# Kernel tuning notes

Hardware: AMD Instinct MI355X
Metric: run time of the kernel (lower is better)

## Reference

```python
import jax, jax.numpy as jnp
import numpy as np

B, T, D, O, E = 4, 4096, 256, 256, 16


def setup_inputs() -> dict:
    key = jax.random.key(0)
    ks = jax.random.split(key, 5)
    s_in = 1.0 / np.sqrt(D)
    x = jax.random.normal(ks[0], (B, T, D), dtype=jnp.float32)
    We = jax.random.uniform(ks[1], (E, D, O), minval=-s_in, maxval=s_in, dtype=jnp.float32)
    be = jax.random.uniform(ks[2], (E, O), minval=-s_in, maxval=s_in, dtype=jnp.float32)
    Wg = jax.random.uniform(ks[3], (D, E), minval=-s_in, maxval=s_in, dtype=jnp.float32)
    bg = jax.random.uniform(ks[4], (E,), minval=-s_in, maxval=s_in, dtype=jnp.float32)
    return {"x": x, "We": We, "be": be, "Wg": Wg, "bg": bg}


def reference(x, We, be, Wg, bg):
    # gate: softmax over experts  [B,T,E]
    gate = jax.nn.softmax(jnp.einsum("btd,de->bte", x, Wg) + bg, axis=-1)
    # all experts: batched GEMM  [B,T,E,O]
    h = jax.nn.gelu(jnp.einsum("btd,edo->bteo", x, We) + be, approximate=False)
    # softmax-weighted sum over experts  [B,T,O]
    return jnp.einsum("bteo,bte->bto", h, gate)
```

## Files before the change

kernel.cpp:

```cpp
#include <hip/hip_runtime.h>
#include <stdint.h>

#define KD 256
#define NO 256
#define NE 16
#define BM 64
#define BN 128
#define XROW 264
#define GROW 68

typedef short bf16x8 __attribute__((ext_vector_type(8)));
typedef float f32x4 __attribute__((ext_vector_type(4)));

__device__ __forceinline__ unsigned short f2bf(float f) {
  uint32_t u = __float_as_uint(f);
  u += 0x7fffu + ((u >> 16) & 1u);
  return (unsigned short)(u >> 16);
}
__device__ __forceinline__ float bf2f(unsigned short h) {
  return __uint_as_float(((uint32_t)h) << 16);
}
__device__ __forceinline__ float gelu_f(float h) {
#if __has_builtin(__builtin_amdgcn_exp2f)
  float zn = h * fmaf(-0.10294817f, h * h, -2.3022077f);
  return h * __builtin_amdgcn_rcpf(1.0f + __builtin_amdgcn_exp2f(zn));
#else
  float z = h * fmaf(0.07135481627f, h * h, 1.5957691216f);
  return h * __builtin_amdgcn_rcpf(1.0f + __expf(-z));
#endif
}

__device__ __forceinline__ void dma16(const void* g, void* l) {
  __builtin_amdgcn_global_load_lds(
      (const __attribute__((address_space(1))) uint32_t*)g,
      (__attribute__((address_space(3))) uint32_t*)l, 16, 0, 0);
}

__global__ void moe_prep(const float* __restrict__ We, unsigned short* __restrict__ Wf,
                         const float* __restrict__ Wg, unsigned short* __restrict__ Wgt)
{
  const int tid = threadIdx.x;
  const int bid = blockIdx.x;
  const int w = tid >> 6, lane = tid & 63;
  const int g = bid * 4 + w;
  const int e = g >> 7, kc = (g >> 4) & 7, ob = g & 15;
  const int q = lane >> 4, ln = lane & 15;

  const float* src = We + ((size_t)e * KD + kc * 32 + q * 8) * NO + ob * 16 + ln;
  unsigned int pk[4];
#pragma unroll
  for (int h = 0; h < 4; ++h) {
    unsigned short lo = f2bf(src[(h * 2 + 0) * NO]);
    unsigned short hi = f2bf(src[(h * 2 + 1) * NO]);
    pk[h] = (unsigned int)lo | ((unsigned int)hi << 16);
  }
  uint4* dst = (uint4*)(Wf + ((((size_t)(e * 8 + kc) * 16 + ob) * 64) + lane) * 8);
  *dst = make_uint4(pk[0], pk[1], pk[2], pk[3]);

  if (bid == 0) {
    int d = tid;
    const float* wr = Wg + (size_t)d * NE;
#pragma unroll
    for (int ee = 0; ee < NE; ++ee)
      Wgt[ee * KD + d] = f2bf(wr[ee]);
  }
}

__launch_bounds__(256, 1)
__global__ void moe_main(const float* __restrict__ x,
                         const uint4* __restrict__ Wf,
                         const unsigned short* __restrict__ Wgt,
                         const float* __restrict__ be,
                         const float* __restrict__ bg,
                         float* __restrict__ out)
{
  __shared__ __align__(16) unsigned char BB[131072];
  __shared__ __align__(16) float gate_t[NE * GROW];
  __shared__ unsigned short be_h[NE * BN];

  unsigned short* const Xs = (unsigned short*)BB;

  const int tid = threadIdx.x;
  const int bid = blockIdx.x;
  const int half = bid & 1;
  const int n0 = half * BN;
  const int m0 = (bid >> 1) * BM;
  const int w = tid >> 6, lane = tid & 63;
  const int ln = lane & 15, quad = lane >> 4;
  const int eoff = __builtin_amdgcn_readfirstlane(((tid >> 6) * 4 + bid) & 15);
  const int obb = half * 8 + w * 2;

  {
    const float4* xg = (const float4*)x + (size_t)m0 * (KD / 4);
#pragma unroll
    for (int p = 0; p < 16; ++p) {
      int idx = p * 256 + tid;
      int r = idx >> 6, c = idx & 63;
      float4 v = xg[r * (KD / 4) + c];
      uint32_t lo = (uint32_t)f2bf(v.x) | ((uint32_t)f2bf(v.y) << 16);
      uint32_t hi = (uint32_t)f2bf(v.z) | ((uint32_t)f2bf(v.w) << 16);
      *(uint2*)&Xs[r * XROW + c * 4] = make_uint2(lo, hi);
    }
  }
#pragma unroll
  for (int p = 0; p < 8; ++p) {
    int idx = p * 256 + tid;
    int e = idx >> 7, c = idx & 127;
    be_h[e * BN + c] = f2bf(be[e * NO + n0 + c]);
  }
  __syncthreads();

  bf16x8 a[4][8];
#pragma unroll
  for (int i = 0; i < 4; ++i)
#pragma unroll
    for (int kc = 0; kc < 8; ++kc)
      a[i][kc] = *(const bf16x8*)&Xs[(i * 16 + ln) * XROW + kc * 32 + quad * 8];

  {
    f32x4 g = {0.f, 0.f, 0.f, 0.f};
#pragma unroll
    for (int kc = 0; kc < 8; ++kc) {
      bf16x8 af = *(const bf16x8*)&Xs[(w * 16 + ln) * XROW + kc * 32 + quad * 8];
      bf16x8 wb = *(const bf16x8*)(Wgt + (size_t)ln * KD + kc * 32 + quad * 8);
      g = __builtin_amdgcn_mfma_f32_16x16x32_bf16(af, wb, g, 0, 0, 0);
    }
    float bgl = bg[ln];
#pragma unroll
    for (int r = 0; r < 4; ++r) {
      float v = g[r] + bgl;
      float mx = v;
#pragma unroll
      for (int msk = 1; msk < 16; msk <<= 1)
        mx = fmaxf(mx, __shfl_xor(mx, msk, 64));
      float ev = __expf(v - mx);
      float s = ev;
#pragma unroll
      for (int msk = 1; msk < 16; msk <<= 1)
        s += __shfl_xor(s, msk, 64);
      gate_t[ln * GROW + w * 16 + quad * 4 + r] = ev * __builtin_amdgcn_rcpf(s);
    }
  }
  __syncthreads();

  const char* const WfB = (const char*)Wf;
  char* const slab0 = (char*)BB + w * 32768;
  char* const slab1 = slab0 + 16384;
  {
    const char* s0 = WfB + (size_t)eoff * 131072 + (size_t)obb * 1024 + lane * 16;
    const char* s1 = WfB + (size_t)((eoff + 1) & 15) * 131072 + (size_t)obb * 1024 + lane * 16;
#pragma unroll
    for (int s = 0; s < 16; ++s)
      dma16(s0 + (s >> 1) * 16384 + (s & 1) * 1024, slab0 + s * 1024 + lane * 16);
#pragma unroll
    for (int s = 0; s < 16; ++s)
      dma16(s1 + (s >> 1) * 16384 + (s & 1) * 1024, slab1 + s * 1024 + lane * 16);
  }

  f32x4 acc[4][2], oacc[4][2];
#pragma unroll
  for (int i = 0; i < 4; ++i)
#pragma unroll
    for (int j = 0; j < 2; ++j) {
      acc[i][j] = (f32x4){0.f, 0.f, 0.f, 0.f};
      oacc[i][j] = (f32x4){0.f, 0.f, 0.f, 0.f};
    }

#pragma unroll 1
  for (int ei = 0; ei < NE; ++ei) {
    const int e = (eoff + ei) & 15;

    if (ei < NE - 1) {
      asm volatile("s_waitcnt vmcnt(16)" ::: "memory");
    } else {
      asm volatile("s_waitcnt vmcnt(0)" ::: "memory");
    }
    __builtin_amdgcn_sched_barrier(0);

    char* const cur = (ei & 1) ? slab1 : slab0;
#pragma unroll
    for (int kc = 0; kc < 8; ++kc) {
      const bf16x8 b0 = *(const bf16x8*)(cur + (kc * 2 + 0) * 1024 + lane * 16);
      const bf16x8 b1 = *(const bf16x8*)(cur + (kc * 2 + 1) * 1024 + lane * 16);
#pragma unroll
      for (int i = 0; i < 4; ++i) {
        acc[i][0] = __builtin_amdgcn_mfma_f32_16x16x32_bf16(a[i][kc], b0, acc[i][0], 0, 0, 0);
        acc[i][1] = __builtin_amdgcn_mfma_f32_16x16x32_bf16(a[i][kc], b1, acc[i][1], 0, 0, 0);
      }
    }

    if (ei < NE - 2) {
      const int en2 = (eoff + ei + 2) & 15;
      const char* sn = WfB + (size_t)en2 * 131072 + (size_t)obb * 1024 + lane * 16;
#pragma unroll
      for (int s = 0; s < 16; ++s)
        dma16(sn + (s >> 1) * 16384 + (s & 1) * 1024, cur + s * 1024 + lane * 16);
    }

    {
      f32x4 gv[4];
#pragma unroll
      for (int i = 0; i < 4; ++i)
        gv[i] = *(const f32x4*)&gate_t[e * GROW + i * 16 + quad * 4];
      const float bb0 = bf2f(be_h[e * BN + w * 32 + ln]);
      const float bb1 = bf2f(be_h[e * BN + w * 32 + 16 + ln]);
#pragma unroll
      for (int i = 0; i < 4; ++i)
#pragma unroll
        for (int j = 0; j < 2; ++j)
#pragma unroll
          for (int r = 0; r < 4; ++r) {
            float hh = acc[i][j][r] + (j ? bb1 : bb0);
            oacc[i][j][r] = fmaf(gv[i][r], gelu_f(hh), oacc[i][j][r]);
            acc[i][j][r] = 0.f;
          }
    }
  }

#pragma unroll
  for (int i = 0; i < 4; ++i)
#pragma unroll
    for (int r = 0; r < 4; ++r) {
      int row = m0 + i * 16 + quad * 4 + r;
      float* orow = out + (size_t)row * NO + n0 + w * 32 + ln;
      orow[0]  = oacc[i][0][r];
      orow[16] = oacc[i][1][r];
    }
}

extern "C" void kernel_launch(void* const* d_in, const int* in_sizes, int n_in,
                              void* d_out, int out_size, void* d_ws, size_t ws_size,
                              hipStream_t stream) {
  const float* x  = (const float*)d_in[0];
  const float* We = (const float*)d_in[1];
  const float* be = (const float*)d_in[2];
  const float* Wg = (const float*)d_in[3];
  const float* bg = (const float*)d_in[4];
  float* out = (float*)d_out;
  unsigned short* Wf  = (unsigned short*)d_ws;
  unsigned short* Wgt = (unsigned short*)((char*)d_ws + (size_t)NE * NO * KD * 2);

  moe_prep<<<512, 256, 0, stream>>>(We, Wf, Wg, Wgt);
  moe_main<<<512, 256, 0, stream>>>(x, (const uint4*)Wf, Wgt, be, bg, out);
}
```

Baseline: 137.3 us.

## Retile MoE kernel to 128x64 blocks with shared cooperative weight slabs

Block tile changes from 64x128 to 128x64, so each wave now owns 32 rows across all 64 columns instead of 64 rows across 32 columns. Expert weight slabs in LDS become shared by all waves, loaded cooperatively (each wave DMAs two k-chunks), which cuts per-block LDS to about 67KB and allows two blocks per CU. This needs workgroup barriers around each expert's compute. B fragments are register double-buffered across k-chunks to hide LDS latency. The trade is less x reuse per weight load and extra barrier sync.

Result: faster. 127.5 us (-7.1%).

```diff
diff --git a/kernel.cpp b/kernel.cpp
--- a/kernel.cpp
+++ b/kernel.cpp
@@ -4,10 +4,10 @@
 #define KD 256
 #define NO 256
 #define NE 16
-#define BM 64
-#define BN 128
+#define BM 128
+#define BN 64
 #define XROW 264
-#define GROW 68
+#define GROW 132
 
 typedef short bf16x8 __attribute__((ext_vector_type(8)));
 typedef float f32x4 __attribute__((ext_vector_type(4)));
@@ -66,7 +66,7 @@
   }
 }
 
-__launch_bounds__(256, 1)
+__launch_bounds__(256, 2)
 __global__ void moe_main(const float* __restrict__ x,
                          const uint4* __restrict__ Wf,
                          const unsigned short* __restrict__ Wgt,
@@ -74,26 +74,26 @@
                          const float* __restrict__ bg,
                          float* __restrict__ out)
 {
-  __shared__ __align__(16) unsigned char BB[131072];
+  __shared__ __align__(16) unsigned char BB[BM * XROW * 2];
   __shared__ __align__(16) float gate_t[NE * GROW];
   __shared__ unsigned short be_h[NE * BN];
 
-  unsigned short* const Xs = (unsigned short*)BB;
-
   const int tid = threadIdx.x;
   const int bid = blockIdx.x;
-  const int half = bid & 1;
-  const int n0 = half * BN;
-  const int m0 = (bid >> 1) * BM;
+  const int cq = bid & 3;
+  const int n0 = cq * BN;
+  const int m0 = (bid >> 2) * BM;
   const int w = tid >> 6, lane = tid & 63;
   const int ln = lane & 15, quad = lane >> 4;
-  const int eoff = __builtin_amdgcn_readfirstlane(((tid >> 6) * 4 + bid) & 15);
-  const int obb = half * 8 + w * 2;
+  const int eoff = __builtin_amdgcn_readfirstlane(bid & 15);
+  const int obBase = cq * 4;
+
+  unsigned short* const Xs = (unsigned short*)BB;
 
   {
     const float4* xg = (const float4*)x + (size_t)m0 * (KD / 4);
 #pragma unroll
-    for (int p = 0; p < 16; ++p) {
+    for (int p = 0; p < 32; ++p) {
       int idx = p * 256 + tid;
       int r = idx >> 6, c = idx & 63;
       float4 v = xg[r * (KD / 4) + c];
@@ -103,25 +103,27 @@
     }
   }
 #pragma unroll
-  for (int p = 0; p < 8; ++p) {
+  for (int p = 0; p < 4; ++p) {
     int idx = p * 256 + tid;
-    int e = idx >> 7, c = idx & 127;
+    int e = idx >> 6, c = idx & 63;
     be_h[e * BN + c] = f2bf(be[e * NO + n0 + c]);
   }
   __syncthreads();
 
-  bf16x8 a[4][8];
-#pragma unroll
-  for (int i = 0; i < 4; ++i)
+  bf16x8 a[2][8];
+#pragma unroll
+  for (int i = 0; i < 2; ++i)
 #pragma unroll
     for (int kc = 0; kc < 8; ++kc)
-      a[i][kc] = *(const bf16x8*)&Xs[(i * 16 + ln) * XROW + kc * 32 + quad * 8];
-
-  {
+      a[i][kc] = *(const bf16x8*)&Xs[(w * 32 + i * 16 + ln) * XROW + kc * 32 + quad * 8];
+
+#pragma unroll
+  for (int pass = 0; pass < 2; ++pass) {
+    const int rw = w * 2 + pass;
     f32x4 g = {0.f, 0.f, 0.f, 0.f};
 #pragma unroll
     for (int kc = 0; kc < 8; ++kc) {
-      bf16x8 af = *(const bf16x8*)&Xs[(w * 16 + ln) * XROW + kc * 32 + quad * 8];
+      bf16x8 af = *(const bf16x8*)&Xs[(rw * 16 + ln) * XROW + kc * 32 + quad * 8];
       bf16x8 wb = *(const bf16x8*)(Wgt + (size_t)ln * KD + kc * 32 + quad * 8);
       g = __builtin_amdgcn_mfma_f32_16x16x32_bf16(af, wb, g, 0, 0, 0);
     }
@@ -138,93 +140,118 @@
 #pragma unroll
       for (int msk = 1; msk < 16; msk <<= 1)
         s += __shfl_xor(s, msk, 64);
-      gate_t[ln * GROW + w * 16 + quad * 4 + r] = ev * __builtin_amdgcn_rcpf(s);
+      gate_t[ln * GROW + rw * 16 + quad * 4 + r] = ev * __builtin_amdgcn_rcpf(s);
     }
   }
   __syncthreads();
 
+  char* const slab0 = (char*)BB;
+  char* const slab1 = (char*)BB + 32768;
   const char* const WfB = (const char*)Wf;
-  char* const slab0 = (char*)BB + w * 32768;
-  char* const slab1 = slab0 + 16384;
   {
-    const char* s0 = WfB + (size_t)eoff * 131072 + (size_t)obb * 1024 + lane * 16;
-    const char* s1 = WfB + (size_t)((eoff + 1) & 15) * 131072 + (size_t)obb * 1024 + lane * 16;
-#pragma unroll
-    for (int s = 0; s < 16; ++s)
-      dma16(s0 + (s >> 1) * 16384 + (s & 1) * 1024, slab0 + s * 1024 + lane * 16);
-#pragma unroll
-    for (int s = 0; s < 16; ++s)
-      dma16(s1 + (s >> 1) * 16384 + (s & 1) * 1024, slab1 + s * 1024 + lane * 16);
-  }
-
-  f32x4 acc[4][2], oacc[4][2];
-#pragma unroll
-  for (int i = 0; i < 4; ++i)
-#pragma unroll
-    for (int j = 0; j < 2; ++j) {
-      acc[i][j] = (f32x4){0.f, 0.f, 0.f, 0.f};
-      oacc[i][j] = (f32x4){0.f, 0.f, 0.f, 0.f};
+    const int e1 = (eoff + 1) & 15;
+#pragma unroll
+    for (int s = 0; s < 8; ++s) {
+      const int kc = w * 2 + (s >> 2), jf = s & 3;
+      dma16(WfB + ((size_t)((eoff * 8 + kc) * 16 + obBase + jf)) * 1024 + lane * 16,
+            slab0 + (kc * 4 + jf) * 1024 + lane * 16);
+    }
+#pragma unroll
+    for (int s = 0; s < 8; ++s) {
+      const int kc = w * 2 + (s >> 2), jf = s & 3;
+      dma16(WfB + ((size_t)((e1 * 8 + kc) * 16 + obBase + jf)) * 1024 + lane * 16,
+            slab1 + (kc * 4 + jf) * 1024 + lane * 16);
+    }
+  }
+
+  f32x4 acc[2][4], oacc[2][4];
+#pragma unroll
+  for (int i = 0; i < 2; ++i)
+#pragma unroll
+    for (int jf = 0; jf < 4; ++jf) {
+      acc[i][jf] = (f32x4){0.f, 0.f, 0.f, 0.f};
+      oacc[i][jf] = (f32x4){0.f, 0.f, 0.f, 0.f};
     }
 
 #pragma unroll 1
   for (int ei = 0; ei < NE; ++ei) {
     const int e = (eoff + ei) & 15;
+    char* const cur = (ei & 1) ? slab1 : slab0;
 
     if (ei < NE - 1) {
-      asm volatile("s_waitcnt vmcnt(16)" ::: "memory");
+      asm volatile("s_waitcnt vmcnt(8)" ::: "memory");
     } else {
       asm volatile("s_waitcnt vmcnt(0)" ::: "memory");
     }
     __builtin_amdgcn_sched_barrier(0);
-
-    char* const cur = (ei & 1) ? slab1 : slab0;
+    __builtin_amdgcn_s_barrier();
+    __builtin_amdgcn_sched_barrier(0);
+
+    bf16x8 bq0[4], bq1[4];
+#pragma unroll
+    for (int jf = 0; jf < 4; ++jf)
+      bq0[jf] = *(const bf16x8*)(cur + jf * 1024 + lane * 16);
 #pragma unroll
     for (int kc = 0; kc < 8; ++kc) {
-      const bf16x8 b0 = *(const bf16x8*)(cur + (kc * 2 + 0) * 1024 + lane * 16);
-      const bf16x8 b1 = *(const bf16x8*)(cur + (kc * 2 + 1) * 1024 + lane * 16);
-#pragma unroll
-      for (int i = 0; i < 4; ++i) {
-        acc[i][0] = __builtin_amdgcn_mfma_f32_16x16x32_bf16(a[i][kc], b0, acc[i][0], 0, 0, 0);
-        acc[i][1] = __builtin_amdgcn_mfma_f32_16x16x32_bf16(a[i][kc], b1, acc[i][1], 0, 0, 0);
+      const bf16x8* cu = (kc & 1) ? bq1 : bq0;
+      bf16x8* nx = (kc & 1) ? bq0 : bq1;
+      if (kc < 7) {
+#pragma unroll
+        for (int jf = 0; jf < 4; ++jf)
+          nx[jf] = *(const bf16x8*)(cur + ((kc + 1) * 4 + jf) * 1024 + lane * 16);
       }
-    }
+#pragma unroll
+      for (int i = 0; i < 2; ++i)
+#pragma unroll
+        for (int jf = 0; jf < 4; ++jf)
+          acc[i][jf] = __builtin_amdgcn_mfma_f32_16x16x32_bf16(
+              a[i][kc], cu[jf], acc[i][jf], 0, 0, 0);
+    }
+
+    __builtin_amdgcn_sched_barrier(0);
+    __builtin_amdgcn_s_barrier();
+    __builtin_amdgcn_sched_barrier(0);
 
     if (ei < NE - 2) {
       const int en2 = (eoff + ei + 2) & 15;
-      const char* sn = WfB + (size_t)en2 * 131072 + (size_t)obb * 1024 + lane * 16;
-#pragma unroll
-      for (int s = 0; s < 16; ++s)
-        dma16(sn + (s >> 1) * 16384 + (s & 1) * 1024, cur + s * 1024 + lane * 16);
+#pragma unroll
+      for (int s = 0; s < 8; ++s) {
+        const int kc = w * 2 + (s >> 2), jf = s & 3;
+        dma16(WfB + ((size_t)((en2 * 8 + kc) * 16 + obBase + jf)) * 1024 + lane * 16,
+              cur + (kc * 4 + jf) * 1024 + lane * 16);
+      }
     }
 
     {
-      f32x4 gv[4];
-#pragma unroll
-      for (int i = 0; i < 4; ++i)
-        gv[i] = *(const f32x4*)&gate_t[e * GROW + i * 16 + quad * 4];
-      const float bb0 = bf2f(be_h[e * BN + w * 32 + ln]);
-      const float bb1 = bf2f(be_h[e * BN + w * 32 + 16 + ln]);
-#pragma unroll
-      for (int i = 0; i < 4; ++i)
-#pragma unroll
-        for (int j = 0; j < 2; ++j)
+      float bbf[4];
+#pragma unroll
+      for (int jf = 0; jf < 4; ++jf)
+        bbf[jf] = bf2f(be_h[e * BN + jf * 16 + ln]);
+#pragma unroll
+      for (int i = 0; i < 2; ++i) {
+        const f32x4 gq = *(const f32x4*)&gate_t[e * GROW + w * 32 + i * 16 + quad * 4];
+#pragma unroll
+        for (int jf = 0; jf < 4; ++jf)
 #pragma unroll
           for (int r = 0; r < 4; ++r) {
-            float hh = acc[i][j][r] + (j ? bb1 : bb0);
-            oacc[i][j][r] = fmaf(gv[i][r], gelu_f(hh), oacc[i][j][r]);
-            acc[i][j][r] = 0.f;
+            float hh = acc[i][jf][r] + bbf[jf];
+            oacc[i][jf][r] = fmaf(gq[r], gelu_f(hh), oacc[i][jf][r]);
+            acc[i][jf][r] = 0.f;
           }
-    }
-  }
-
-#pragma unroll
-  for (int i = 0; i < 4; ++i)
+      }
+    }
+  }
+
+#pragma unroll
+  for (int i = 0; i < 2; ++i)
 #pragma unroll
     for (int r = 0; r < 4; ++r) {
-      int row = m0 + i * 16 + quad * 4 + r;
-      float* orow = out + (size_t)row * NO + n0 + w * 32 + ln;
+      int row = m0 + w * 32 + i * 16 + quad * 4 + r;
+      float* orow = out + (size_t)row * NO + n0 + ln;
       orow[0]  = oacc[i][0][r];
       orow[16] = oacc[i][1][r];
+      orow[32] = oacc[i][2][r];
+      orow[48] = oacc[i][3][r];
     }
 }
 
```
